# Kernel optimization log

Hardware: AMD Instinct MI355X
Metric: run time of the kernel (lower is better)

Reference implementation:

```python
import jax, jax.numpy as jnp
import numpy as np
import math

B, T, C = 2, 2048, 1024
H, DK, DV = 16, 64, 64


def setup_inputs() -> dict:
    key = jax.random.key(0)
    ks = jax.random.split(key, 5)
    # randw(*d) = randn(*d) / sqrt(d[-1])
    x = jax.random.normal(ks[0], (B, T, C), dtype=jnp.float32)
    w_q = jax.random.normal(ks[1], (H, DK, C), dtype=jnp.float32) / math.sqrt(C)
    w_k = jax.random.normal(ks[2], (H, DK, C), dtype=jnp.float32) / math.sqrt(C)
    w_v = jax.random.normal(ks[3], (H, DV, C), dtype=jnp.float32) / math.sqrt(C)
    w_o = jax.random.normal(ks[4], (H * DV, C), dtype=jnp.float32) / math.sqrt(C)
    return {"x": x, "w_q": w_q, "w_k": w_k, "w_v": w_v, "w_o": w_o}


def reference(x, w_q, w_k, w_v, w_o):
    # Full prefill: bs_q.first = 0, bs_q.nb = T, causal=True, dropout=0 (eval).
    dk = w_q.shape[1]
    q = jnp.einsum('ntc,hdc->nhtd', x, w_q)  # [B,H,T,DK]
    k = jnp.einsum('ntc,hdc->nhtd', x, w_k)  # [B,H,T,DK]
    v = jnp.einsum('ntc,hdc->nhtd', x, w_v)  # [B,H,T,DV]
    a = jnp.einsum('nhtd,nhsd->nhts', q, k) / jnp.sqrt(jnp.asarray(dk, x.dtype))
    # amm_generator: mask where query_idx < key_idx (strict upper triangle)
    t = a.shape[-1]
    mask = jnp.arange(t)[:, None] < jnp.arange(t)[None, :]  # [T,T] bool
    a = jnp.where(mask[None, None], jnp.asarray(-jnp.inf, a.dtype), a)
    a = jax.nn.softmax(a, axis=-1)
    y = jnp.einsum('nhts,nhsd->nthd', a, v)  # [B,T,H,DV]
    y = y.reshape(y.shape[0], y.shape[1], -1)  # [B,T,H*DV]
    return y @ w_o  # [B,T,C]
```

## Files before the change

kernel.cpp:

```cpp
#include <hip/hip_runtime.h>
#include <hip/hip_bf16.h>

#define B_ 2
#define T_ 2048
#define C_ 1024
#define H_ 16
#define D_ 64

typedef __attribute__((ext_vector_type(8))) short bf16x8;
typedef __attribute__((ext_vector_type(4))) float f32x4;
typedef __attribute__((ext_vector_type(16))) float f32x16;
typedef __attribute__((ext_vector_type(8))) unsigned short u16x8;
typedef __attribute__((ext_vector_type(2))) unsigned int u32x2;
typedef __attribute__((ext_vector_type(4))) unsigned int u32x4;

__device__ __forceinline__ unsigned short bf1(float a) {
    __bf16 x = (__bf16)a;
    return __builtin_bit_cast(unsigned short, x);
}
__device__ __forceinline__ unsigned int pk2(float a, float b) {
    return (unsigned int)bf1(a) | ((unsigned int)bf1(b) << 16);
}
__device__ __forceinline__ float bf2f(unsigned short u) {
    union { unsigned int u; float f; } v; v.u = (unsigned int)u << 16;
    return v.f;
}

__device__ __forceinline__ void gll16(const void* g, void* l) {
    __builtin_amdgcn_global_load_lds(
        (const __attribute__((address_space(1))) unsigned int*)g,
        (__attribute__((address_space(3))) unsigned int*)l, 16, 0, 0);
}

__global__ __launch_bounds__(256) void prep_all(
    const float* __restrict__ x, const float* __restrict__ wq,
    const float* __restrict__ wk, const float* __restrict__ wv,
    unsigned short* __restrict__ xb, unsigned short* __restrict__ wb)
{
    const int bid = blockIdx.x, tid = threadIdx.x;
    if (bid < 1024) {
        const size_t i = ((size_t)bid * 256 + tid) * 16;
        float4 f0 = *reinterpret_cast<const float4*>(x + i);
        float4 f1 = *reinterpret_cast<const float4*>(x + i + 4);
        float4 f2 = *reinterpret_cast<const float4*>(x + i + 8);
        float4 f3 = *reinterpret_cast<const float4*>(x + i + 12);
        u32x4 a = {pk2(f0.x, f0.y), pk2(f0.z, f0.w), pk2(f1.x, f1.y), pk2(f1.z, f1.w)};
        u32x4 b = {pk2(f2.x, f2.y), pk2(f2.z, f2.w), pk2(f3.x, f3.y), pk2(f3.z, f3.w)};
        *reinterpret_cast<u32x4*>(xb + i) = a;
        *reinterpret_cast<u32x4*>(xb + i + 8) = b;
    } else {
        const int rb = (bid - 1024) * 4;
        const float* src = (rb < 1024) ? wq + (size_t)rb * 1024
                         : (rb < 2048) ? wk + (size_t)(rb - 1024) * 1024
                                       : wv + (size_t)(rb - 2048) * 1024;
        const float sc = (rb < 1024) ? 0.125f * 1.4426950408889634f : 1.0f;
        const float4* s4 = (const float4*)src;
        u32x2* d = (u32x2*)(wb + (size_t)rb * 1024);
#pragma unroll
        for (int k = 0; k < 4; k++) {
            float4 v = s4[k * 256 + tid];
            u32x2 w;
            w[0] = pk2(v.x * sc, v.y * sc);
            w[1] = pk2(v.z * sc, v.w * sc);
            d[k * 256 + tid] = w;
        }
    }
}

__global__ __launch_bounds__(256) void qkv_gemm(
    const unsigned short* __restrict__ xb, const unsigned short* __restrict__ wb,
    unsigned short* __restrict__ qkv)
{
    __shared__ __align__(16) unsigned short As[128 * 32];
    __shared__ __align__(16) unsigned short Bs[128 * 32];
    const int tid = threadIdx.x;
    const int lane = tid & 63, wave = tid >> 6;
    const int g = lane >> 4, c16 = lane & 15;
    const int xcd = blockIdx.x & 7, idx = blockIdx.x >> 3;
    const int bm = (xcd << 2) + idx / 24, bn = idx % 24;
    const int jbase = bn << 7;
    const int which = jbase >> 10;

    const int srow = lane >> 2, sch = (lane & 3) << 3;
    const unsigned short* asrc = xb + ((size_t)(bm << 7) + wave * 32 + srow) * C_ + sch;
    const unsigned short* bsrc = wb + ((size_t)(bn << 7) + wave * 32 + srow) * C_ + sch;

    f32x4 acc[4][4];
#pragma unroll
    for (int i = 0; i < 4; i++)
#pragma unroll
        for (int j = 0; j < 4; j++) acc[i][j] = (f32x4){0.f, 0.f, 0.f, 0.f};

    const int wm = (wave >> 1) << 6, wn = (wave & 1) << 6;

    for (int t = 0; t < 32; ++t) {
        const int k0 = t << 5;
        __syncthreads();
        gll16(asrc + k0,           &As[(wave * 32) << 5]);
        gll16(asrc + k0 + 16 * C_, &As[(wave * 32 + 16) << 5]);
        gll16(bsrc + k0,           &Bs[(wave * 32) << 5]);
        gll16(bsrc + k0 + 16 * C_, &Bs[(wave * 32 + 16) << 5]);
        __syncthreads();

        bf16x8 af[4], bfv[4];
#pragma unroll
        for (int m = 0; m < 4; m++)
            af[m] = *reinterpret_cast<const bf16x8*>(&As[((wm + m * 16 + c16) << 5) + g * 8]);
#pragma unroll
        for (int n = 0; n < 4; n++)
            bfv[n] = *reinterpret_cast<const bf16x8*>(&Bs[((wn + n * 16 + c16) << 5) + g * 8]);
#pragma unroll
        for (int m = 0; m < 4; m++)
#pragma unroll
            for (int n = 0; n < 4; n++)
                acc[m][n] = __builtin_amdgcn_mfma_f32_16x16x32_bf16(af[m], bfv[n], acc[m][n], 0, 0, 0);
    }

    if (which < 2) {
#pragma unroll
        for (int m = 0; m < 4; m++) {
            const int grow = (bm << 7) + wm + m * 16 + (g << 2);
#pragma unroll
            for (int n = 0; n < 4; n++) {
                const int jj = (jbase + wn + n * 16 + c16) & 1023;
                const int h = jj >> 6, d = jj & 63;
#pragma unroll
                for (int r = 0; r < 4; r++) {
                    const int row = grow + r;
                    const int b = row >> 11, t = row & 2047;
                    const size_t off = ((size_t)((which * B_ + b) * H_ + h) * T_ + t) * 64 + d;
                    qkv[off] = bf1(acc[m][n][r]);
                }
            }
        }
    } else {
#pragma unroll
        for (int m = 0; m < 4; m++) {
            const int grow = (bm << 7) + wm + m * 16 + (g << 2);
            const int b = grow >> 11, t = grow & 2047;
#pragma unroll
            for (int n = 0; n < 4; n++) {
                const int jj = (jbase + wn + n * 16 + c16) & 1023;
                const int h = jj >> 6, d = jj & 63;
                u32x2 w;
                w[0] = pk2(acc[m][n][0], acc[m][n][1]);
                w[1] = pk2(acc[m][n][2], acc[m][n][3]);
                const size_t off = ((size_t)((2 * B_ + b) * H_ + h) * 64 + d) * T_ + t;
                *reinterpret_cast<u32x2*>(&qkv[off]) = w;
            }
        }
    }
}

__global__ __launch_bounds__(256) void attn(
    const unsigned short* __restrict__ qkv,
    unsigned short* __restrict__ opA, unsigned short* __restrict__ opB,
    float* __restrict__ lbuf)
{
    __shared__ __align__(16) unsigned short Ks[64 * 64];
    __shared__ __align__(16) unsigned short Vt[64 * 64];
    __shared__ __align__(16) unsigned short Ps[4][32 * 64];
    const int tid = threadIdx.x, lane = tid & 63, w = tid >> 6;
    const int l31 = lane & 31, lh = lane >> 5;
    const int qt = 15 - (blockIdx.x >> 6);
    const int rem = blockIdx.x & 63;
    const int split = rem >> 5, bh = rem & 31;
    const int b = bh >> 4, h = bh & 15;
    const size_t headoff = (size_t)(b * H_ + h) * T_ * 64;
    const size_t QSZ = (size_t)B_ * H_ * T_ * 64;
    const unsigned short* qp = qkv + headoff;
    const unsigned short* kp = qkv + QSZ + headoff;
    const unsigned short* vTp = qkv + 2 * QSZ + headoff;

    const int itlo = split ? (qt + 1) : 0;
    const int ithi = split ? (2 * qt + 2) : (qt + 1);

    const int qb = (qt << 7) + w * 32;
    const int qg = qb + l31;

    bf16x8 qf[4];
#pragma unroll
    for (int f = 0; f < 4; f++)
        qf[f] = *reinterpret_cast<const bf16x8*>(qp + (size_t)qg * 64 + f * 16 + lh * 8);

    f32x16 oacc[2];
#pragma unroll
    for (int i = 0; i < 16; i++) { oacc[0][i] = 0.f; oacc[1][i] = 0.f; }
    float l_lane = 0.f;

    const int cx = l31 & 7;
    const unsigned short* kbase = Ks + (l31 << 6);
    const unsigned short* vbase = Vt + (l31 << 6);
    const unsigned short* prb = Ps[w] + (l31 << 6);
    unsigned short* pwb = Ps[w] + (l31 << 6);

    const int srow8 = lane >> 3;
    const int swc = ((lane & 7) ^ srow8) << 3;
    const unsigned short* ksrc = kp + (size_t)(w * 16 + srow8) * 64 + swc;
    const unsigned short* vsrc = vTp + (size_t)(w * 16 + srow8) * T_ + swc;

    for (int it = itlo; it < ithi; ++it) {
        const int s0 = it << 6;
        __syncthreads();
#pragma unroll
        for (int i = 0; i < 2; i++) {
            gll16(ksrc + (size_t)(s0 + i * 8) * 64, &Ks[(w * 16 + i * 8) << 6]);
            gll16(vsrc + s0 + (size_t)i * 8 * T_, &Vt[(w * 16 + i * 8) << 6]);
        }
        __syncthreads();

        if (s0 > qb + 31) continue;

        f32x16 sq[2];
#pragma unroll
        for (int i = 0; i < 16; i++) { sq[0][i] = -16.f; sq[1][i] = -16.f; }
        __builtin_amdgcn_s_setprio(1);
#pragma unroll
        for (int kf = 0; kf < 2; kf++) {
#pragma unroll
            for (int f = 0; f < 4; f++) {
                bf16x8 ka = *reinterpret_cast<const bf16x8*>(
                    kbase + (kf << 11) + ((((f << 1) + lh) ^ cx) << 3));
                sq[kf] = __builtin_amdgcn_mfma_f32_32x32x16_bf16(ka, qf[f], sq[kf], 0, 0, 0);
            }
        }
        __builtin_amdgcn_s_setprio(0);

        if (s0 + 63 > qb) {
#pragma unroll
            for (int kf = 0; kf < 2; kf++)
#pragma unroll
                for (int r = 0; r < 16; r++) {
                    const int kv = s0 + (kf << 5) + (r & 3) + ((r >> 2) << 3) + (lh << 2);
                    if (kv > qg) sq[kf][r] = -1e30f;
                }
        }

#pragma unroll
        for (int kf = 0; kf < 2; kf++)
#pragma unroll
            for (int r = 0; r < 16; r++) {
                const float pv = __builtin_amdgcn_exp2f(sq[kf][r]);
                sq[kf][r] = pv;
                l_lane += pv;
            }

#pragma unroll
        for (int kf = 0; kf < 2; kf++)
#pragma unroll
            for (int rr = 0; rr < 4; rr++) {
                u32x2 wv;
                wv[0] = pk2(sq[kf][4 * rr], sq[kf][4 * rr + 1]);
                wv[1] = pk2(sq[kf][4 * rr + 2], sq[kf][4 * rr + 3]);
                *reinterpret_cast<u32x2*>(
                    pwb + ((((kf << 2) + rr) ^ cx) << 3) + (lh << 2)) = wv;
            }

        bf16x8 pB[4];
#pragma unroll
        for (int kf2 = 0; kf2 < 4; kf2++)
            pB[kf2] = *reinterpret_cast<const bf16x8*>(
                prb + ((((kf2 << 1) + lh) ^ cx) << 3));
        __builtin_amdgcn_s_setprio(1);
#pragma unroll
        for (int df = 0; df < 2; df++) {
#pragma unroll
            for (int kf2 = 0; kf2 < 4; kf2++) {
                bf16x8 va = *reinterpret_cast<const bf16x8*>(
                    vbase + (df << 11) + ((((kf2 << 1) + lh) ^ cx) << 3));
                oacc[df] = __builtin_amdgcn_mfma_f32_32x32x16_bf16(va, pB[kf2], oacc[df], 0, 0, 0);
            }
        }
        __builtin_amdgcn_s_setprio(0);
    }

    unsigned short* op = split ? opB : opA;
    const size_t orow = ((size_t)b * T_ + qg) * 1024 + h * 64;
#pragma unroll
    for (int df = 0; df < 2; df++)
#pragma unroll
        for (int rr = 0; rr < 4; rr++) {
            const int d = (df << 5) + (rr << 3) + (lh << 2);
            u32x2 wv;
            wv[0] = pk2(oacc[df][4 * rr], oacc[df][4 * rr + 1]);
            wv[1] = pk2(oacc[df][4 * rr + 2], oacc[df][4 * rr + 3]);
            *reinterpret_cast<u32x2*>(&op[orow + d]) = wv;
        }
    l_lane += __shfl_xor(l_lane, 32, 64);
    if (lane < 32)
        lbuf[(size_t)split * (B_ * H_ * T_) + ((size_t)(b * H_ + h)) * T_ + qg] = l_lane;
}

__global__ __launch_bounds__(256) void combine_wo(
    const unsigned short* __restrict__ opA, const unsigned short* __restrict__ opB,
    const float* __restrict__ lbuf, unsigned short* __restrict__ y,
    const float* __restrict__ wo, unsigned short* __restrict__ wt)
{
    __shared__ unsigned short tile[64][72];
    const int bid = blockIdx.x, tid = threadIdx.x;
    if (bid < 2048) {
        const size_t i = ((size_t)bid * 256 + tid) * 8;
        const int hh = (int)((i >> 6) & 15);
        const int t = (int)((i >> 10) & 2047);
        const int bb = (int)(i >> 21);
        const size_t li = ((size_t)(bb * H_ + hh)) * T_ + t;
        const float inv = 1.0f / (lbuf[li] + lbuf[(size_t)B_ * H_ * T_ + li]);
        u16x8 a = *reinterpret_cast<const u16x8*>(opA + i);
        u16x8 c = *reinterpret_cast<const u16x8*>(opB + i);
        unsigned short o[8];
#pragma unroll
        for (int j = 0; j < 8; j++) o[j] = bf1((bf2f(a[j]) + bf2f(c[j])) * inv);
        *reinterpret_cast<u16x8*>(y + i) = *reinterpret_cast<u16x8*>(o);
    } else {
        const int wb2 = bid - 2048;
        const int tk = (wb2 & 15) << 6, tn = (wb2 >> 4) << 6;
        const int r = tid >> 2, cb = (tid & 3) << 4;
#pragma unroll
        for (int j = 0; j < 4; j++) {
            float4 v = *reinterpret_cast<const float4*>(
                wo + (size_t)(tk + r) * 1024 + tn + cb + j * 4);
            u32x2 w;
            w[0] = pk2(v.x, v.y);
            w[1] = pk2(v.z, v.w);
            *reinterpret_cast<u32x2*>(&tile[r][cb + j * 4]) = w;
        }
        __syncthreads();
        unsigned short buf[16];
#pragma unroll
        for (int j = 0; j < 16; j++) buf[j] = tile[cb + j][r];
        unsigned short* dst = wt + (size_t)(tn + r) * 1024 + tk + cb;
        *reinterpret_cast<u16x8*>(dst) = *reinterpret_cast<u16x8*>(buf);
        *reinterpret_cast<u16x8*>(dst + 8) = *reinterpret_cast<u16x8*>(buf + 8);
    }
}

__global__ __launch_bounds__(256) void out_proj(
    const unsigned short* __restrict__ y, const unsigned short* __restrict__ wt,
    float* __restrict__ out)
{
    __shared__ __align__(16) unsigned short As[128 * 32];
    __shared__ __align__(16) unsigned short Bs[64 * 32];
    const int tid = threadIdx.x;
    const int lane = tid & 63, wave = tid >> 6;
    const int g = lane >> 4, c16 = lane & 15;
    const int xcd = blockIdx.x & 7, idx = blockIdx.x >> 3;
    const int bm = (xcd << 2) + (idx >> 4), bn = idx & 15;
    const int wm = (wave >> 1) << 6, wn = (wave & 1) << 5;

    const int srow = lane >> 2, sch = (lane & 3) << 3;
    const unsigned short* ysrc = y + ((size_t)(bm << 7) + wave * 32 + srow) * 1024 + sch;
    const unsigned short* wsrc = wt + ((size_t)(bn << 6) + wave * 16 + srow) * 1024 + sch;

    f32x4 acc[4][2];
#pragma unroll
    for (int i = 0; i < 4; i++)
#pragma unroll
        for (int j = 0; j < 2; j++) acc[i][j] = (f32x4){0.f, 0.f, 0.f, 0.f};

    for (int t = 0; t < 32; ++t) {
        const int k0 = t << 5;
        __syncthreads();
        gll16(ysrc + k0,             &As[(wave * 32) << 5]);
        gll16(ysrc + k0 + 16 * 1024, &As[(wave * 32 + 16) << 5]);
        gll16(wsrc + k0,             &Bs[(wave * 16) << 5]);
        __syncthreads();

        bf16x8 af[4], bfr[2];
#pragma unroll
        for (int m = 0; m < 4; m++)
            af[m] = *reinterpret_cast<const bf16x8*>(&As[((wm + m * 16 + c16) << 5) + g * 8]);
#pragma unroll
        for (int n = 0; n < 2; n++)
            bfr[n] = *reinterpret_cast<const bf16x8*>(&Bs[((wn + n * 16 + c16) << 5) + g * 8]);
#pragma unroll
        for (int m = 0; m < 4; m++)
#pragma unroll
            for (int n = 0; n < 2; n++)
                acc[m][n] = __builtin_amdgcn_mfma_f32_16x16x32_bf16(af[m], bfr[n], acc[m][n], 0, 0, 0);
    }

#pragma unroll
    for (int m = 0; m < 4; m++) {
        const int grow = (bm << 7) + wm + m * 16 + (g << 2);
#pragma unroll
        for (int n = 0; n < 2; n++) {
            const int gcol = (bn << 6) + wn + n * 16 + c16;
#pragma unroll
            for (int r = 0; r < 4; r++)
                out[(size_t)(grow + r) * 1024 + gcol] = acc[m][n][r];
        }
    }
}

extern "C" void kernel_launch(void* const* d_in, const int* in_sizes, int n_in,
                              void* d_out, int out_size, void* d_ws, size_t ws_size,
                              hipStream_t stream) {
    const float* x  = (const float*)d_in[0];
    const float* wq = (const float*)d_in[1];
    const float* wk = (const float*)d_in[2];
    const float* wv = (const float*)d_in[3];
    const float* wo = (const float*)d_in[4];
    float* out = (float*)d_out;

    unsigned short* wb   = (unsigned short*)d_ws;
    unsigned short* opB  = (unsigned short*)d_ws;
    unsigned short* y    = opB;
    unsigned short* qkv  = (unsigned short*)d_ws + (size_t)4 * 1024 * 1024;
    unsigned short* wt   = qkv;
    unsigned short* xb   = (unsigned short*)d_out;
    unsigned short* opA  = (unsigned short*)d_out;
    float* lbuf = (float*)((char*)d_out + (size_t)8 * 1024 * 1024);

    prep_all<<<dim3(1792), 256, 0, stream>>>(x, wq, wk, wv, xb, wb);
    qkv_gemm<<<dim3(768), 256, 0, stream>>>(xb, wb, qkv);
    attn<<<dim3(1024), 256, 0, stream>>>(qkv, opA, opB, lbuf);
    combine_wo<<<dim3(2048 + 256), 256, 0, stream>>>(opA, opB, lbuf, y, wo, wt);
    out_proj<<<dim3(512), 256, 0, stream>>>(y, wt, out);
}
```

Before: 107.5 us.

## Prepack K/V in MFMA fragment order and drop LDS staging in attention

The projection kernel now writes K and V in a tile-packed layout that matches the MFMA operand fragments, so each attention wave loads its K/V fragments straight from global memory with contiguous 16-byte loads. The LDS buffers, both block-wide barriers per tile, and the P round trip through LDS go away. P is rearranged into the B operand with cross-half-wave shuffles instead. Each wave now stops at its own causal limit and blocks are reordered to group heads, likely for L2 locality. The cost is that every wave fetches K/V from global or cache independently rather than sharing one LDS copy, and register pressure rises from holding 16 fragment vectors.

```diff
diff --git a/kernel.cpp b/kernel.cpp
--- a/kernel.cpp
+++ b/kernel.cpp
@@ -24,6 +24,9 @@
 __device__ __forceinline__ float bf2f(unsigned short u) {
     union { unsigned int u; float f; } v; v.u = (unsigned int)u << 16;
     return v.f;
+}
+__device__ __forceinline__ unsigned int sx32(unsigned int v) {
+    return (unsigned int)__shfl_xor((int)v, 32, 64);
 }
 
 __device__ __forceinline__ void gll16(const void* g, void* l) {
@@ -116,7 +119,7 @@
                 acc[m][n] = __builtin_amdgcn_mfma_f32_16x16x32_bf16(af[m], bfv[n], acc[m][n], 0, 0, 0);
     }
 
-    if (which < 2) {
+    if (which == 0) {
 #pragma unroll
         for (int m = 0; m < 4; m++) {
             const int grow = (bm << 7) + wm + m * 16 + (g << 2);
@@ -128,24 +131,49 @@
                 for (int r = 0; r < 4; r++) {
                     const int row = grow + r;
                     const int b = row >> 11, t = row & 2047;
-                    const size_t off = ((size_t)((which * B_ + b) * H_ + h) * T_ + t) * 64 + d;
+                    const size_t off = ((size_t)(b * H_ + h) * T_ + t) * 64 + d;
                     qkv[off] = bf1(acc[m][n][r]);
                 }
             }
         }
-    } else {
+    } else if (which == 1) {
 #pragma unroll
         for (int m = 0; m < 4; m++) {
             const int grow = (bm << 7) + wm + m * 16 + (g << 2);
-            const int b = grow >> 11, t = grow & 2047;
 #pragma unroll
             for (int n = 0; n < 4; n++) {
                 const int jj = (jbase + wn + n * 16 + c16) & 1023;
                 const int h = jj >> 6, d = jj & 63;
+                const int f = d >> 4, lhk = (d >> 3) & 1, j = d & 7;
+#pragma unroll
+                for (int r = 0; r < 4; r++) {
+                    const int row = grow + r;
+                    const int b = row >> 11, tt = row & 2047;
+                    const size_t off = ((size_t)((B_ + b) * H_ + h) * T_) * 64
+                        + ((size_t)(tt >> 6) << 12)
+                        + ((((((tt >> 5) & 1) << 2) + f)) << 9)
+                        + (((lhk << 5) + (tt & 31)) << 3) + j;
+                    qkv[off] = bf1(acc[m][n][r]);
+                }
+            }
+        }
+    } else {
+#pragma unroll
+        for (int m = 0; m < 4; m++) {
+            const int grow = (bm << 7) + wm + m * 16 + (g << 2);
+            const int b = grow >> 11, tt = grow & 2047;
+            const int tau = tt >> 6, kf2 = (tt >> 4) & 3, lhv = (tt >> 3) & 1, jb = tt & 7;
+#pragma unroll
+            for (int n = 0; n < 4; n++) {
+                const int jj = (jbase + wn + n * 16 + c16) & 1023;
+                const int h = jj >> 6, d = jj & 63;
+                const int df = d >> 5, l31v = d & 31;
                 u32x2 w;
                 w[0] = pk2(acc[m][n][0], acc[m][n][1]);
                 w[1] = pk2(acc[m][n][2], acc[m][n][3]);
-                const size_t off = ((size_t)((2 * B_ + b) * H_ + h) * 64 + d) * T_ + t;
+                const size_t off = ((size_t)((2 * B_ + b) * H_ + h) * T_) * 64
+                    + ((size_t)tau << 12) + (((df << 2) + kf2) << 9)
+                    + (((lhv << 5) + l31v) << 3) + jb;
                 *reinterpret_cast<u32x2*>(&qkv[off]) = w;
             }
         }
@@ -157,27 +185,28 @@
     unsigned short* __restrict__ opA, unsigned short* __restrict__ opB,
     float* __restrict__ lbuf)
 {
-    __shared__ __align__(16) unsigned short Ks[64 * 64];
-    __shared__ __align__(16) unsigned short Vt[64 * 64];
-    __shared__ __align__(16) unsigned short Ps[4][32 * 64];
     const int tid = threadIdx.x, lane = tid & 63, w = tid >> 6;
     const int l31 = lane & 31, lh = lane >> 5;
-    const int qt = 15 - (blockIdx.x >> 6);
-    const int rem = blockIdx.x & 63;
-    const int split = rem >> 5, bh = rem & 31;
+    const int xs = blockIdx.x & 7;
+    const int inner = blockIdx.x >> 3;
+    const int qt = 15 - (inner >> 3);
+    const int split = (inner >> 2) & 1;
+    const int bh = (xs << 2) + (inner & 3);
     const int b = bh >> 4, h = bh & 15;
     const size_t headoff = (size_t)(b * H_ + h) * T_ * 64;
     const size_t QSZ = (size_t)B_ * H_ * T_ * 64;
     const unsigned short* qp = qkv + headoff;
-    const unsigned short* kp = qkv + QSZ + headoff;
-    const unsigned short* vTp = qkv + 2 * QSZ + headoff;
-
-    const int itlo = split ? (qt + 1) : 0;
-    const int ithi = split ? (2 * qt + 2) : (qt + 1);
+    const unsigned short* kpk = qkv + QSZ + headoff;
+    const unsigned short* vpk = qkv + 2 * QSZ + headoff;
 
     const int qb = (qt << 7) + w * 32;
     const int qg = qb + l31;
 
+    const int itlo = split ? (qt + 1) : 0;
+    const int ithi_blk = split ? (2 * qt + 2) : (qt + 1);
+    const int wave_hi = (qb + 31) >> 6;
+    const int ithi = min(ithi_blk, wave_hi + 1);
+
     bf16x8 qf[4];
 #pragma unroll
     for (int f = 0; f < 4; f++)
@@ -188,45 +217,39 @@
     for (int i = 0; i < 16; i++) { oacc[0][i] = 0.f; oacc[1][i] = 0.f; }
     float l_lane = 0.f;
 
-    const int cx = l31 & 7;
-    const unsigned short* kbase = Ks + (l31 << 6);
-    const unsigned short* vbase = Vt + (l31 << 6);
-    const unsigned short* prb = Ps[w] + (l31 << 6);
-    unsigned short* pwb = Ps[w] + (l31 << 6);
-
-    const int srow8 = lane >> 3;
-    const int swc = ((lane & 7) ^ srow8) << 3;
-    const unsigned short* ksrc = kp + (size_t)(w * 16 + srow8) * 64 + swc;
-    const unsigned short* vsrc = vTp + (size_t)(w * 16 + srow8) * T_ + swc;
+    const int lo16 = lane << 3;
 
     for (int it = itlo; it < ithi; ++it) {
         const int s0 = it << 6;
-        __syncthreads();
-#pragma unroll
-        for (int i = 0; i < 2; i++) {
-            gll16(ksrc + (size_t)(s0 + i * 8) * 64, &Ks[(w * 16 + i * 8) << 6]);
-            gll16(vsrc + s0 + (size_t)i * 8 * T_, &Vt[(w * 16 + i * 8) << 6]);
-        }
-        __syncthreads();
-
-        if (s0 > qb + 31) continue;
+        const unsigned short* kt = kpk + ((size_t)it << 12);
+        const unsigned short* vt = vpk + ((size_t)it << 12);
+
+        bf16x8 ka[2][4], va[2][4];
+#pragma unroll
+        for (int kf = 0; kf < 2; kf++)
+#pragma unroll
+            for (int f = 0; f < 4; f++)
+                ka[kf][f] = *reinterpret_cast<const bf16x8*>(
+                    kt + ((((kf << 2) + f)) << 9) + lo16);
+#pragma unroll
+        for (int df = 0; df < 2; df++)
+#pragma unroll
+            for (int kf2 = 0; kf2 < 4; kf2++)
+                va[df][kf2] = *reinterpret_cast<const bf16x8*>(
+                    vt + ((((df << 2) + kf2)) << 9) + lo16);
 
         f32x16 sq[2];
 #pragma unroll
         for (int i = 0; i < 16; i++) { sq[0][i] = -16.f; sq[1][i] = -16.f; }
         __builtin_amdgcn_s_setprio(1);
 #pragma unroll
-        for (int kf = 0; kf < 2; kf++) {
-#pragma unroll
-            for (int f = 0; f < 4; f++) {
-                bf16x8 ka = *reinterpret_cast<const bf16x8*>(
-                    kbase + (kf << 11) + ((((f << 1) + lh) ^ cx) << 3));
-                sq[kf] = __builtin_amdgcn_mfma_f32_32x32x16_bf16(ka, qf[f], sq[kf], 0, 0, 0);
-            }
-        }
+        for (int kf = 0; kf < 2; kf++)
+#pragma unroll
+            for (int f = 0; f < 4; f++)
+                sq[kf] = __builtin_amdgcn_mfma_f32_32x32x16_bf16(ka[kf][f], qf[f], sq[kf], 0, 0, 0);
         __builtin_amdgcn_s_setprio(0);
 
-        if (s0 + 63 > qb) {
+        if (it == wave_hi) {
 #pragma unroll
             for (int kf = 0; kf < 2; kf++)
 #pragma unroll
@@ -245,32 +268,31 @@
                 l_lane += pv;
             }
 
+        bf16x8 pB[4];
 #pragma unroll
         for (int kf = 0; kf < 2; kf++)
 #pragma unroll
-            for (int rr = 0; rr < 4; rr++) {
-                u32x2 wv;
-                wv[0] = pk2(sq[kf][4 * rr], sq[kf][4 * rr + 1]);
-                wv[1] = pk2(sq[kf][4 * rr + 2], sq[kf][4 * rr + 3]);
-                *reinterpret_cast<u32x2*>(
-                    pwb + ((((kf << 2) + rr) ^ cx) << 3) + (lh << 2)) = wv;
+            for (int bq = 0; bq < 2; bq++) {
+                const unsigned int A0 = pk2(sq[kf][8 * bq + 0], sq[kf][8 * bq + 1]);
+                const unsigned int B0 = pk2(sq[kf][8 * bq + 2], sq[kf][8 * bq + 3]);
+                const unsigned int A1 = pk2(sq[kf][8 * bq + 4], sq[kf][8 * bq + 5]);
+                const unsigned int B1 = pk2(sq[kf][8 * bq + 6], sq[kf][8 * bq + 7]);
+                const unsigned int A0s = sx32(A0), B0s = sx32(B0);
+                const unsigned int A1s = sx32(A1), B1s = sx32(B1);
+                u32x4 wv;
+                wv[0] = lh ? A1s : A0;
+                wv[1] = lh ? B1s : B0;
+                wv[2] = lh ? A1 : A0s;
+                wv[3] = lh ? B1 : B0s;
+                pB[(kf << 1) + bq] = __builtin_bit_cast(bf16x8, wv);
             }
 
-        bf16x8 pB[4];
-#pragma unroll
-        for (int kf2 = 0; kf2 < 4; kf2++)
-            pB[kf2] = *reinterpret_cast<const bf16x8*>(
-                prb + ((((kf2 << 1) + lh) ^ cx) << 3));
         __builtin_amdgcn_s_setprio(1);
 #pragma unroll
-        for (int df = 0; df < 2; df++) {
-#pragma unroll
-            for (int kf2 = 0; kf2 < 4; kf2++) {
-                bf16x8 va = *reinterpret_cast<const bf16x8*>(
-                    vbase + (df << 11) + ((((kf2 << 1) + lh) ^ cx) << 3));
-                oacc[df] = __builtin_amdgcn_mfma_f32_32x32x16_bf16(va, pB[kf2], oacc[df], 0, 0, 0);
-            }
-        }
+        for (int df = 0; df < 2; df++)
+#pragma unroll
+            for (int kf2 = 0; kf2 < 4; kf2++)
+                oacc[df] = __builtin_amdgcn_mfma_f32_32x32x16_bf16(va[df][kf2], pB[kf2], oacc[df], 0, 0, 0);
         __builtin_amdgcn_s_setprio(0);
     }
 
```

Result: slower. 109.8 us (+2.1%).
